# Performance work log

Hardware: AMD Instinct MI355X
Metric: run time of the kernel (lower is better)

## Reference

```python
import jax, jax.numpy as jnp
import numpy as np

N_USERS, N_ITEMS = 100000, 50000
DIM = 128
E_U, E_I = 400000, 200000
B = 4096


def _init_layer(key, dim):
    k1, k2, k3 = jax.random.split(key, 3)
    s = 1.0 / np.sqrt(dim)
    W = jax.random.uniform(k1, (dim, dim), jnp.float32, -s, s)
    a_src = jax.random.uniform(k2, (dim,), jnp.float32, -s, s)
    a_dst = jax.random.uniform(k3, (dim,), jnp.float32, -s, s)
    return W, a_src, a_dst


def setup_inputs() -> dict:
    key = jax.random.key(0)
    ks = jax.random.split(key, 12)
    inp = {
        "uedg_index": jax.random.randint(ks[0], (2, E_U), 0, N_USERS),
        "iedg_index": jax.random.randint(ks[1], (2, E_I), 0, N_ITEMS),
        "user_id": jax.random.randint(ks[2], (B,), 0, N_USERS),
        "item_id": jax.random.randint(ks[3], (B,), 0, N_ITEMS),
        "uedg_value": jax.random.uniform(ks[4], (E_U,), jnp.float32),
        "iedg_value": jax.random.uniform(ks[5], (E_I,), jnp.float32),
        # learned parameters (t.rand init in the original)
        "user_matrix": jax.random.uniform(ks[6], (N_USERS, DIM), jnp.float32),
        "item_matrix": jax.random.uniform(ks[7], (N_ITEMS, DIM), jnp.float32),
    }
    for name, k in (("u1", ks[8]), ("u2", ks[9]), ("i1", ks[10]), ("i2", ks[11])):
        W, a_s, a_d = _init_layer(k, DIM)
        inp[f"W_{name}"] = W
        inp[f"a_src_{name}"] = a_s
        inp[f"a_dst_{name}"] = a_d
    return inp


def gat_layer(x, edge_index, edge_value, W, a_src, a_dst):
    """Single-head GAT layer with per-edge weights (dropout disabled / eval mode)."""
    n = x.shape[0]
    h = x @ W                                   # [N, D]
    src, dst = edge_index[0], edge_index[1]
    hs, hd = h[src], h[dst]                     # [E, D] gathers
    logits = jax.nn.leaky_relu((hs * a_src).sum(-1) + (hd * a_dst).sum(-1), 0.2)  # [E]
    # numerically-stable neighbor softmax over destination nodes
    m = jax.ops.segment_max(logits, dst, num_segments=n)
    e = jnp.exp(logits - m[dst]) * edge_value
    denom = jax.ops.segment_sum(e, dst, num_segments=n)
    coef = e / (denom[dst] + 1e-16)
    out = jax.ops.segment_sum(hs * coef[:, None], dst, num_segments=n)  # scatter-add aggregation
    return jax.nn.elu(out)


def reference(uedg_index, iedg_index, user_id, item_id, uedg_value, iedg_value,
              user_matrix, item_matrix,
              W_u1, a_src_u1, a_dst_u1, W_u2, a_src_u2, a_dst_u2,
              W_i1, a_src_i1, a_dst_i1, W_i2, a_src_i2, a_dst_i2):
    iout = gat_layer(item_matrix, iedg_index, iedg_value, W_i1, a_src_i1, a_dst_i1)
    uout = gat_layer(user_matrix, uedg_index, uedg_value, W_u1, a_src_u1, a_dst_u1)
    iout = gat_layer(iout, iedg_index, iedg_value, W_i2, a_src_i2, a_dst_i2)
    uout = gat_layer(uout, uedg_index, uedg_value, W_u2, a_src_u2, a_dst_u2)
    user_vc = uout[user_id]   # index_select over rows
    item_vc = iout[item_id]
    return user_vc, item_vc
```

## Files before the change

kernel.cpp:

```cpp
#include <hip/hip_runtime.h>
#include <hip/hip_bf16.h>

#define DIM 128
#define KSEG 32

typedef short bf16x8 __attribute__((ext_vector_type(8)));
typedef float f32x4  __attribute__((ext_vector_type(4)));

__device__ __forceinline__ float elu_f(float x) { return x > 0.f ? x : expm1f(x); }

__device__ __forceinline__ unsigned short f2bfu(float f) {
    return __builtin_bit_cast(unsigned short, __float2bfloat16(f));
}
__device__ __forceinline__ float bf2f(unsigned short b) {
    return __uint_as_float(((unsigned)b) << 16);
}

struct PrepArgs {
    const float* W[4];
    const float* as[4];
    const float* ad[4];
    unsigned short* Wt;
    unsigned short* wa;
};

__global__ __launch_bounds__(256) void init_all(int* __restrict__ z, int n, PrepArgs p, int nz)
{
    const int t = threadIdx.x;
    if ((int)blockIdx.x < nz) {
        int i = blockIdx.x * 256 + t;
        if (i < n) z[i] = 0;
        return;
    }
    __shared__ float as[DIM], ad[DIM];
    __shared__ float sr[4][2];
    const int pb    = blockIdx.x - nz;
    const int layer = pb >> 3;
    const int blk   = pb & 7;
    const float* W  = p.W[layer];
    unsigned short* W_t = p.Wt + layer * DIM * DIM;
    unsigned short* wa  = p.wa + layer * 2 * DIM;
    if (t < DIM) as[t] = p.as[layer][t];
    else ad[t - DIM] = p.ad[layer][t - DIM];
    __syncthreads();
    const int half = t >> 7;
    const int c = t & 127;
    const int wv = t >> 6;
    const int k_end = blk * 16 + 16;
    for (int k0 = blk * 16; k0 < k_end; k0 += 2) {
        const int k = k0 + half;
        float w = W[k * DIM + c];
        W_t[c * DIM + k] = f2bfu(w);
        float vs = w * as[c], vd = w * ad[c];
#pragma unroll
        for (int o = 32; o > 0; o >>= 1) { vs += __shfl_down(vs, o); vd += __shfl_down(vd, o); }
        if ((t & 63) == 0) { sr[wv][0] = vs; sr[wv][1] = vd; }
        __syncthreads();
        if (t < 2) {
            const int kk = k0 + t;
            wa[kk]       = f2bfu(sr[2 * t][0] + sr[2 * t + 1][0]);
            wa[DIM + kk] = f2bfu(sr[2 * t][1] + sr[2 * t + 1][1]);
        }
        __syncthreads();
    }
}

__global__ __launch_bounds__(256) void mark_isB(const int* __restrict__ uid, const int* __restrict__ iid,
                                                int B, int NU, int* __restrict__ isB, int* __restrict__ flag)
{
    int ent = blockIdx.x * 256 + threadIdx.x;
    if (ent >= 2 * B) return;
    int n = (ent < B) ? uid[ent] : NU + iid[ent - B];
    isB[n] = 1;
    flag[n] = 1;
}

__global__ __launch_bounds__(256) void pass1_gemm(
    const int* __restrict__ ued, const int* __restrict__ ied,
    const float* __restrict__ uval, const float* __restrict__ ival,
    int EU, int EI, const int* __restrict__ isB, int* __restrict__ flag,
    int* __restrict__ cnt, int2* __restrict__ epair,
    const float* __restrict__ xu, const float* __restrict__ xi,
    const unsigned short* __restrict__ Wt_u, const unsigned short* __restrict__ Wt_i,
    const unsigned short* __restrict__ wa_u, const unsigned short* __restrict__ wa_i,
    unsigned short* __restrict__ h, float* __restrict__ s_src, float* __restrict__ s_dst,
    int NU, int NI, int gu)
{
    __shared__ short xs[2][64 * 128];
    const int t = threadIdx.x;

    const int gbid = blockIdx.x;
    const bool isU = gbid < gu;
    const int b0   = isU ? gbid : gbid - gu;
    const int nblk = isU ? gu : (gridDim.x - gu);
    const int Nl   = isU ? NU : NI;
    const int gofs = isU ? 0 : NU;
    const float* xf = isU ? xu : xi;
    const unsigned short* W_t = isU ? Wt_u : Wt_i;
    const unsigned short* wa  = isU ? wa_u : wa_i;
    const int ntiles = (Nl + 63) >> 6;

    int srow[4], suc[4];
#pragma unroll
    for (int i = 0; i < 4; ++i) {
        int unit = i * 256 + t;
        srow[i] = unit >> 4;
        suc[i]  = unit & 15;
    }
    float4 va[4], vb[4];

    auto LOADREGS = [&](int r0) {
#pragma unroll
        for (int i = 0; i < 4; ++i) {
            int gr = r0 + srow[i];
            if (gr < Nl) {
                const float4* p = reinterpret_cast<const float4*>(&xf[(size_t)gr * DIM + suc[i] * 8]);
                va[i] = p[0];
                vb[i] = p[1];
            } else {
                va[i] = make_float4(0.f, 0.f, 0.f, 0.f);
                vb[i] = make_float4(0.f, 0.f, 0.f, 0.f);
            }
        }
    };
    auto STORELDS = [&](int buf) {
#pragma unroll
        for (int i = 0; i < 4; ++i) {
            bf16x8 bv;
            bv[0] = (short)f2bfu(va[i].x); bv[1] = (short)f2bfu(va[i].y);
            bv[2] = (short)f2bfu(va[i].z); bv[3] = (short)f2bfu(va[i].w);
            bv[4] = (short)f2bfu(vb[i].x); bv[5] = (short)f2bfu(vb[i].y);
            bv[6] = (short)f2bfu(vb[i].z); bv[7] = (short)f2bfu(vb[i].w);
            int byte = srow[i] * 256 + ((suc[i] * 16) ^ ((srow[i] & 7) << 4));
            *reinterpret_cast<bf16x8*>(reinterpret_cast<char*>(xs[buf]) + byte) = bv;
        }
    };

    const bool hasTile = b0 < ntiles;
    if (hasTile) LOADREGS(b0 * 64);

    {
        const int ET = EU + EI;
        const int stride = gridDim.x * 256;
        int e0 = gbid * 256 + t;
        int nd[4], sv[4]; float vv[4]; int ib[4];
#pragma unroll
        for (int j = 0; j < 4; ++j) {
            int e = e0 + j * stride;
            nd[j] = -1;
            if (e < ET) {
                if (e < EU) { nd[j] = ued[EU + e]; sv[j] = ued[e]; vv[j] = uval[e]; }
                else { int ee = e - EU; nd[j] = NU + ied[EI + ee]; sv[j] = NU + ied[ee]; vv[j] = ival[ee]; }
            }
        }
#pragma unroll
        for (int j = 0; j < 4; ++j)
            ib[j] = (nd[j] >= 0) ? isB[nd[j]] : 0;
#pragma unroll
        for (int j = 0; j < 4; ++j) {
            if (ib[j]) {
                int rk = atomicAdd(&cnt[nd[j]], 1);
                if (rk < KSEG)
                    epair[(size_t)nd[j] * KSEG + rk] = make_int2(sv[j], __float_as_int(vv[j]));
                flag[sv[j]] = 1;
            }
        }
    }

    if (!hasTile) return;

    const int wv = t >> 6;
    const int l  = t & 63;
    const int lo = l & 15;
    const int hi = l >> 4;

    bf16x8 wf[4][2];
#pragma unroll
    for (int cb2 = 0; cb2 < 2; ++cb2) {
        const unsigned short* base = W_t + (wv * 32 + cb2 * 16 + lo) * DIM + hi * 8;
#pragma unroll
        for (int kb = 0; kb < 4; ++kb)
            wf[kb][cb2] = *reinterpret_cast<const bf16x8*>(base + kb * 32);
    }
    bf16x8 sfrag[4];
    if (lo < 2) {
        const unsigned short* sb = wa + lo * DIM + hi * 8;
#pragma unroll
        for (int kb = 0; kb < 4; ++kb)
            sfrag[kb] = *reinterpret_cast<const bf16x8*>(sb + kb * 32);
    } else {
#pragma unroll
        for (int kb = 0; kb < 4; ++kb) {
            bf16x8 z = { 0, 0, 0, 0, 0, 0, 0, 0 };
            sfrag[kb] = z;
        }
    }

    int tile = b0;
    STORELDS(0);
    __syncthreads();
    int cur = 0;
    for (;;) {
        const int nextTile = tile + nblk;
        const bool more = nextTile < ntiles;
        if (more) LOADREGS(nextTile * 64);

        const int r0 = tile * 64;
#pragma unroll
        for (int rb = 0; rb < 4; ++rb) {
            const int arow = rb * 16 + lo;
            bf16x8 a[4];
#pragma unroll
            for (int kb = 0; kb < 4; ++kb) {
                int byte = arow * 256 + ((kb * 64 + hi * 16) ^ ((arow & 7) << 4));
                a[kb] = *reinterpret_cast<const bf16x8*>(reinterpret_cast<const char*>(xs[cur]) + byte);
            }
            f32x4 acc0 = {0.f,0.f,0.f,0.f}, acc1 = {0.f,0.f,0.f,0.f};
#pragma unroll
            for (int kb = 0; kb < 4; ++kb) {
                acc0 = __builtin_amdgcn_mfma_f32_16x16x32_bf16(a[kb], wf[kb][0], acc0, 0, 0, 0);
                acc1 = __builtin_amdgcn_mfma_f32_16x16x32_bf16(a[kb], wf[kb][1], acc1, 0, 0, 0);
            }
#pragma unroll
            for (int i = 0; i < 4; ++i) {
                int row = r0 + rb * 16 + hi * 4 + i;
                if (row < Nl) {
                    size_t grow = (size_t)(gofs + row);
                    h[grow * DIM + wv * 32 + lo]      = f2bfu(acc0[i]);
                    h[grow * DIM + wv * 32 + 16 + lo] = f2bfu(acc1[i]);
                }
            }
            if (rb == wv) {
                f32x4 acc_s = {0.f,0.f,0.f,0.f};
#pragma unroll
                for (int kb = 0; kb < 4; ++kb)
                    acc_s = __builtin_amdgcn_mfma_f32_16x16x32_bf16(a[kb], sfrag[kb], acc_s, 0, 0, 0);
#pragma unroll
                for (int i = 0; i < 4; ++i) {
                    int row = r0 + wv * 16 + hi * 4 + i;
                    if (row < Nl) {
                        if (lo == 0) s_src[gofs + row] = acc_s[i];
                        else if (lo == 1) s_dst[gofs + row] = acc_s[i];
                    }
                }
            }
        }

        if (!more) break;
        STORELDS(cur ^ 1);
        __syncthreads();
        cur ^= 1;
        tile = nextTile;
    }
}

__global__ __launch_bounds__(256) void pass2_scan(
    const int* __restrict__ ued, const int* __restrict__ ied,
    const float* __restrict__ uval, const float* __restrict__ ival,
    int EU, int EI, const int* __restrict__ isB, const int* __restrict__ flag,
    int* __restrict__ cnt, int2* __restrict__ epair, int gP,
    int NT, int* __restrict__ aux, int NU)
{
    const int t = threadIdx.x;
    if ((int)blockIdx.x < gP) {
        const int ET = EU + EI;
        const int stride = gP * 256;
        int e0 = blockIdx.x * 256 + t;
        int nd[4], sv[4]; float vv[4]; int act[4];
#pragma unroll
        for (int j = 0; j < 4; ++j) {
            int e = e0 + j * stride;
            nd[j] = -1;
            if (e < ET) {
                if (e < EU) { nd[j] = ued[EU + e]; sv[j] = ued[e]; vv[j] = uval[e]; }
                else { int ee = e - EU; nd[j] = NU + ied[EI + ee]; sv[j] = NU + ied[ee]; vv[j] = ival[ee]; }
            }
        }
#pragma unroll
        for (int j = 0; j < 4; ++j)
            act[j] = (nd[j] >= 0) ? (flag[nd[j]] && !isB[nd[j]]) : 0;
#pragma unroll
        for (int j = 0; j < 4; ++j) {
            if (act[j]) {
                int rk = atomicAdd(&cnt[nd[j]], 1);
                if (rk < KSEG)
                    epair[(size_t)nd[j] * KSEG + rk] = make_int2(sv[j], __float_as_int(vv[j]));
            }
        }
        return;
    }
    __shared__ int sm[4];
    int i = (blockIdx.x - gP) * 256 + t;
    int v = (i < NT) ? flag[i] : 0;
#pragma unroll
    for (int o = 32; o > 0; o >>= 1) v += __shfl_down(v, o);
    if ((t & 63) == 0) sm[t >> 6] = v;
    __syncthreads();
    if (t == 0) aux[blockIdx.x - gP] = sm[0] + sm[1] + sm[2] + sm[3];
}

__global__ __launch_bounds__(256) void scan_build(const int* __restrict__ flag, const int* __restrict__ aux,
                                                  int NT, int NU, int nb,
                                                  int* __restrict__ alist, int* __restrict__ cpos,
                                                  int* __restrict__ hdr)
{
    __shared__ int s[256];
    __shared__ int sm[16];
    const int t = threadIdx.x;
    const int b = blockIdx.x;
    const int i = b * 256 + t;
    int v = (i < NT) ? flag[i] : 0;
    s[t] = v;
    __syncthreads();
    for (int o = 1; o < 256; o <<= 1) {
        int u = (t >= o) ? s[t - o] : 0;
        __syncthreads();
        s[t] += u;
        __syncthreads();
    }

    const int bNU = NU >> 8, oNU = NU & 255;
    int pb = 0, pn = 0, pt = 0;
    for (int j = t; j < nb; j += 256) {
        int av = aux[j];
        if (j < b)   pb += av;
        if (j < bNU) pn += av;
        pt += av;
    }
#pragma unroll
    for (int o = 32; o > 0; o >>= 1) {
        pb += __shfl_down(pb, o);
        pn += __shfl_down(pn, o);
        pt += __shfl_down(pt, o);
    }
    int r = (t < oNU) ? flag[bNU * 256 + t] : 0;
#pragma unroll
    for (int o = 32; o > 0; o >>= 1) r += __shfl_down(r, o);
    if ((t & 63) == 0) {
        int w = t >> 6;
        sm[w] = pb; sm[4 + w] = pn; sm[8 + w] = pt; sm[12 + w] = r;
    }
    __syncthreads();
    const int exb = sm[0] + sm[1] + sm[2] + sm[3];
    const int nau = sm[4] + sm[5] + sm[6] + sm[7] + sm[12] + sm[13] + sm[14] + sm[15];
    const int na  = sm[8] + sm[9] + sm[10] + sm[11];
    const int nau_pad = (nau + 63) & ~63;
    const int nap = nau_pad + (na - nau);
    const int excl = exb + s[t] - v;

    if (i < NT && v) {
        int pos = (i < NU) ? excl : nau_pad + (excl - nau);
        alist[pos] = i;
        cpos[i] = pos;
    }
    if (b == 0) {
        if (t == 0) { hdr[0] = nau; hdr[1] = na; }
        if (t < 64) {
            int ss = nau + t;
            if (ss < nau_pad) alist[ss] = -1;
        } else if (t < 128) {
            alist[nap + (t - 64)] = -1;
        }
    }
}

__global__ __launch_bounds__(256) void csr_agg_act(const int* __restrict__ cnt, const int2* __restrict__ epair,
                                                   const float* __restrict__ ssrc, const float* __restrict__ sdst,
                                                   const unsigned short* __restrict__ h,
                                                   unsigned short* __restrict__ outb,
                                                   const int* __restrict__ alist, const int* __restrict__ hdr)
{
    const int nau = hdr[0], na = hdr[1];
    const int nap = ((nau + 63) & ~63) + (na - nau);
    int g = (blockIdx.x * 256 + threadIdx.x) >> 4;
    int l16 = threadIdx.x & 15;
    if (g >= nap) return;
    int n = alist[g];
    if (n < 0) return;
    const size_t beg = (size_t)n * KSEG;
    int md = min(cnt[n], KSEG);
    float sd = sdst[n];
    float m = -INFINITY, den = 0.f;
    float acc[8] = {0,0,0,0,0,0,0,0};
    for (int base = 0; base < md; base += 16) {
        int c16 = min(16, md - base);
        int sidx = 0; float l = -INFINITY, evv = 0.f;
        if (l16 < c16) {
            int2 pr = epair[beg + base + l16];
            sidx = pr.x;
            evv = __int_as_float(pr.y);
            float ll = ssrc[sidx] + sd;
            l = ll >= 0.f ? ll : 0.2f * ll;
        }
        float cm = l;
#pragma unroll
        for (int o = 8; o > 0; o >>= 1) cm = fmaxf(cm, __shfl_xor(cm, o, 16));
        float nm = fmaxf(m, cm);
        float sc = __expf(m - nm);
        den *= sc;
#pragma unroll
        for (int j = 0; j < 8; ++j) acc[j] *= sc;
        float p = (l16 < c16) ? __expf(l - nm) * evv : 0.f;
        float ps = p;
#pragma unroll
        for (int o = 8; o > 0; o >>= 1) ps += __shfl_xor(ps, o, 16);
        den += ps;
        for (int k0 = 0; k0 < c16; k0 += 4) {
            bf16x8 hv[4]; float cc[4];
#pragma unroll
            for (int j = 0; j < 4; ++j) {
                int k = k0 + j;
                cc[j] = 0.f;
                if (k < c16) {
                    cc[j] = __shfl(p, k, 16);
                    int s = __shfl(sidx, k, 16);
                    hv[j] = *reinterpret_cast<const bf16x8*>(&h[(size_t)s * DIM + l16 * 8]);
                }
            }
#pragma unroll
            for (int j = 0; j < 4; ++j) {
                if (k0 + j < c16) {
#pragma unroll
                    for (int q = 0; q < 8; ++q)
                        acc[q] = fmaf(bf2f((unsigned short)hv[j][q]), cc[j], acc[q]);
                }
            }
        }
        m = nm;
    }
    float inv = 1.f / (den + 1e-16f);
    bf16x8 o;
#pragma unroll
    for (int q = 0; q < 8; ++q) o[q] = (short)f2bfu(elu_f(acc[q] * inv));
    *reinterpret_cast<bf16x8*>(&outb[(size_t)n * DIM + l16 * 8]) = o;
}

__global__ __launch_bounds__(256) void gemm_act(const unsigned short* __restrict__ xbb,
                                                const unsigned short* __restrict__ Wt_u,
                                                const unsigned short* __restrict__ Wt_i,
                                                const unsigned short* __restrict__ wa_u,
                                                const unsigned short* __restrict__ wa_i,
                                                unsigned short* __restrict__ h, float* __restrict__ s_src,
                                                float* __restrict__ s_dst,
                                                const int* __restrict__ alist, const int* __restrict__ hdr)
{
    const int nau = hdr[0], na = hdr[1];
    const int nau_pad = (nau + 63) & ~63;
    const int nap = nau_pad + (na - nau);
    const int r0 = blockIdx.x * 64;
    if (r0 >= nap) return;

    __shared__ short xs[64 * 128];
    __shared__ int rowid[64];
    const int t  = threadIdx.x;
    const int wv = t >> 6;
    const int l  = t & 63;
    const int lo = l & 15;
    const int hi = l >> 4;

    const bool isU = r0 < nau_pad;
    const unsigned short* W_t = isU ? Wt_u : Wt_i;
    const unsigned short* wa  = isU ? wa_u : wa_i;

    if (t < 64) rowid[t] = alist[r0 + t];
    __syncthreads();

    bf16x8 wf[4][2];
#pragma unroll
    for (int cb2 = 0; cb2 < 2; ++cb2) {
        const unsigned short* base = W_t + (wv * 32 + cb2 * 16 + lo) * DIM + hi * 8;
#pragma unroll
        for (int kb = 0; kb < 4; ++kb)
            wf[kb][cb2] = *reinterpret_cast<const bf16x8*>(base + kb * 32);
    }
    bf16x8 sfrag[4];
    if (lo < 2) {
        const unsigned short* sb = wa + lo * DIM + hi * 8;
#pragma unroll
        for (int kb = 0; kb < 4; ++kb)
            sfrag[kb] = *reinterpret_cast<const bf16x8*>(sb + kb * 32);
    } else {
#pragma unroll
        for (int kb = 0; kb < 4; ++kb) {
            bf16x8 z = { 0, 0, 0, 0, 0, 0, 0, 0 };
            sfrag[kb] = z;
        }
    }

#pragma unroll
    for (int i = 0; i < 4; ++i) {
        int unit = i * 256 + t;
        int row = unit >> 4, uc = unit & 15;
        int node = rowid[row];
        bf16x8 bv = { 0, 0, 0, 0, 0, 0, 0, 0 };
        if (node >= 0)
            bv = *reinterpret_cast<const bf16x8*>(&xbb[(size_t)node * DIM + uc * 8]);
        int byte = row * 256 + ((uc * 16) ^ ((row & 7) << 4));
        *reinterpret_cast<bf16x8*>(reinterpret_cast<char*>(xs) + byte) = bv;
    }
    __syncthreads();

#pragma unroll
    for (int rb = 0; rb < 4; ++rb) {
        const int arow = rb * 16 + lo;
        bf16x8 a[4];
#pragma unroll
        for (int kb = 0; kb < 4; ++kb) {
            int byte = arow * 256 + ((kb * 64 + hi * 16) ^ ((arow & 7) << 4));
            a[kb] = *reinterpret_cast<const bf16x8*>(reinterpret_cast<const char*>(xs) + byte);
        }
        f32x4 acc0 = {0.f,0.f,0.f,0.f}, acc1 = {0.f,0.f,0.f,0.f};
#pragma unroll
        for (int kb = 0; kb < 4; ++kb) {
            acc0 = __builtin_amdgcn_mfma_f32_16x16x32_bf16(a[kb], wf[kb][0], acc0, 0, 0, 0);
            acc1 = __builtin_amdgcn_mfma_f32_16x16x32_bf16(a[kb], wf[kb][1], acc1, 0, 0, 0);
        }
#pragma unroll
        for (int i = 0; i < 4; ++i) {
            int row = rb * 16 + hi * 4 + i;
            if (rowid[row] >= 0) {
                size_t grow = (size_t)(r0 + row);
                h[grow * DIM + wv * 32 + lo]      = f2bfu(acc0[i]);
                h[grow * DIM + wv * 32 + 16 + lo] = f2bfu(acc1[i]);
            }
        }
        if (rb == wv) {
            f32x4 acc_s = {0.f,0.f,0.f,0.f};
#pragma unroll
            for (int kb = 0; kb < 4; ++kb)
                acc_s = __builtin_amdgcn_mfma_f32_16x16x32_bf16(a[kb], sfrag[kb], acc_s, 0, 0, 0);
#pragma unroll
            for (int i = 0; i < 4; ++i) {
                int row = wv * 16 + hi * 4 + i;
                if (rowid[row] >= 0) {
                    if (lo == 0) s_src[r0 + row] = acc_s[i];
                    else if (lo == 1) s_dst[r0 + row] = acc_s[i];
                }
            }
        }
    }
}

__global__ __launch_bounds__(256) void csr_agg_batch(const int* __restrict__ cnt, const int2* __restrict__ epair,
                                                     const float* __restrict__ ssrc, const float* __restrict__ sdst,
                                                     const unsigned short* __restrict__ h,
                                                     const int* __restrict__ cpos,
                                                     const int* __restrict__ uid, const int* __restrict__ iid,
                                                     float* __restrict__ out, int B, int NU)
{
    int ent = (blockIdx.x * 256 + threadIdx.x) >> 4;
    int l16 = threadIdx.x & 15;
    if (ent >= 2 * B) return;
    int n = (ent < B) ? uid[ent] : NU + iid[ent - B];
    const size_t beg = (size_t)n * KSEG;
    int md = min(cnt[n], KSEG);
    float sd = sdst[cpos[n]];
    float m = -INFINITY, den = 0.f;
    float acc[8] = {0,0,0,0,0,0,0,0};
    for (int base = 0; base < md; base += 16) {
        int c16 = min(16, md - base);
        int cps = 0; float l = -INFINITY, evv = 0.f;
        if (l16 < c16) {
            int2 pr = epair[beg + base + l16];
            cps = cpos[pr.x];
            evv = __int_as_float(pr.y);
            float ll = ssrc[cps] + sd;
            l = ll >= 0.f ? ll : 0.2f * ll;
        }
        float cm = l;
#pragma unroll
        for (int o = 8; o > 0; o >>= 1) cm = fmaxf(cm, __shfl_xor(cm, o, 16));
        float nm = fmaxf(m, cm);
        float sc = __expf(m - nm);
        den *= sc;
#pragma unroll
        for (int j = 0; j < 8; ++j) acc[j] *= sc;
        float p = (l16 < c16) ? __expf(l - nm) * evv : 0.f;
        float ps = p;
#pragma unroll
        for (int o = 8; o > 0; o >>= 1) ps += __shfl_xor(ps, o, 16);
        den += ps;
        for (int k0 = 0; k0 < c16; k0 += 4) {
            bf16x8 hv[4]; float cc[4];
#pragma unroll
            for (int j = 0; j < 4; ++j) {
                int k = k0 + j;
                cc[j] = 0.f;
                if (k < c16) {
                    cc[j] = __shfl(p, k, 16);
                    int s = __shfl(cps, k, 16);
                    hv[j] = *reinterpret_cast<const bf16x8*>(&h[(size_t)s * DIM + l16 * 8]);
                }
            }
#pragma unroll
            for (int j = 0; j < 4; ++j) {
                if (k0 + j < c16) {
#pragma unroll
                    for (int q = 0; q < 8; ++q)
                        acc[q] = fmaf(bf2f((unsigned short)hv[j][q]), cc[j], acc[q]);
                }
            }
        }
        m = nm;
    }
    float inv = 1.f / (den + 1e-16f);
    float4 o0 = { elu_f(acc[0]*inv), elu_f(acc[1]*inv), elu_f(acc[2]*inv), elu_f(acc[3]*inv) };
    float4 o1 = { elu_f(acc[4]*inv), elu_f(acc[5]*inv), elu_f(acc[6]*inv), elu_f(acc[7]*inv) };
    float4* op = reinterpret_cast<float4*>(&out[(size_t)ent * DIM + l16 * 8]);
    op[0] = o0;
    op[1] = o1;
}

extern "C" void kernel_launch(void* const* d_in, const int* in_sizes, int n_in,
                              void* d_out, int out_size, void* d_ws, size_t ws_size,
                              hipStream_t stream)
{
    const int*   uedg    = (const int*)d_in[0];
    const int*   iedg    = (const int*)d_in[1];
    const int*   user_id = (const int*)d_in[2];
    const int*   item_id = (const int*)d_in[3];
    const float* uval    = (const float*)d_in[4];
    const float* ival    = (const float*)d_in[5];
    const float* umat    = (const float*)d_in[6];
    const float* imat    = (const float*)d_in[7];
    const float* W_u1 = (const float*)d_in[8];
    const float* as_u1 = (const float*)d_in[9];
    const float* ad_u1 = (const float*)d_in[10];
    const float* W_u2 = (const float*)d_in[11];
    const float* as_u2 = (const float*)d_in[12];
    const float* ad_u2 = (const float*)d_in[13];
    const float* W_i1 = (const float*)d_in[14];
    const float* as_i1 = (const float*)d_in[15];
    const float* ad_i1 = (const float*)d_in[16];
    const float* W_i2 = (const float*)d_in[17];
    const float* as_i2 = (const float*)d_in[18];
    const float* ad_i2 = (const float*)d_in[19];

    const int EU = in_sizes[0] / 2;
    const int EI = in_sizes[1] / 2;
    const int B  = in_sizes[2];
    const int NU = in_sizes[6] / DIM;
    const int NI = in_sizes[7] / DIM;
    const int NT = NU + NI;
    const int ET = EU + EI;
    const int nb = (NT + 255) / 256;

    unsigned short* h    = (unsigned short*)d_ws;
    unsigned short* Wt_a = h + (size_t)NT * DIM;
    unsigned short* wa_a = Wt_a + 4 * DIM * DIM;
    unsigned short* xbb  = wa_a + 4 * 2 * DIM;
    float* ssrc   = (float*)(xbb + (size_t)NT * DIM);
    float* sdst   = ssrc + NT;
    int2*  epair  = (int2*)(sdst + NT);
    int*   cnt    = (int*)(epair + (size_t)NT * KSEG);
    int*   flag   = cnt + NT;
    int*   isB    = flag + NT;
    int*   hdr    = isB + NT;
    int*   aux    = hdr + 8;
    int*   alist  = aux + 1024;
    int*   cpos   = alist + (NT + 128);

    PrepArgs pa;
    pa.W[0] = W_u1; pa.W[1] = W_u2; pa.W[2] = W_i1; pa.W[3] = W_i2;
    pa.as[0] = as_u1; pa.as[1] = as_u2; pa.as[2] = as_i1; pa.as[3] = as_i2;
    pa.ad[0] = ad_u1; pa.ad[1] = ad_u2; pa.ad[2] = ad_i1; pa.ad[3] = ad_i2;
    pa.Wt = Wt_a; pa.wa = wa_a;

    const int zn = 3 * NT;
    const int nz = (zn + 255) / 256;
    init_all<<<nz + 32, 256, 0, stream>>>(cnt, zn, pa, nz);

    mark_isB<<<(2 * B + 255) / 256, 256, 0, stream>>>(user_id, item_id, B, NU, isB, flag);

    const int gu = 512, gi = 256;
    pass1_gemm<<<gu + gi, 256, 0, stream>>>(
        uedg, iedg, uval, ival, EU, EI, isB, flag, cnt, epair,
        umat, imat, Wt_a + 0 * DIM * DIM, Wt_a + 2 * DIM * DIM,
        wa_a + 0 * 2 * DIM, wa_a + 2 * 2 * DIM, h, ssrc, sdst, NU, NI, gu);

    const int gP = (ET + 1023) / 1024;
    pass2_scan<<<gP + nb, 256, 0, stream>>>(uedg, iedg, uval, ival, EU, EI, isB, flag, cnt, epair, gP,
                                            NT, aux, NU);

    scan_build<<<nb, 256, 0, stream>>>(flag, aux, NT, NU, nb, alist, cpos, hdr);

    csr_agg_act<<<(NT + 128 + 15) / 16, 256, 0, stream>>>(cnt, epair, ssrc, sdst, h, xbb, alist, hdr);

    gemm_act<<<(NT + 192) / 64, 256, 0, stream>>>(xbb,
        Wt_a + 1 * DIM * DIM, Wt_a + 3 * DIM * DIM, wa_a + 1 * 2 * DIM, wa_a + 3 * 2 * DIM,
        h, ssrc, sdst, alist, hdr);

    csr_agg_batch<<<(2 * B * 16 + 255) / 256, 256, 0, stream>>>(cnt, epair, ssrc, sdst, h, cpos,
        user_id, item_id, (float*)d_out, B, NU);
}
```

Measured before the change: 92.69 us.

## Replace persistent double-buffered projection GEMM with one 128-row tile per block

The first-layer projection kernel no longer loops over 64-row tiles with a register prefetch and double-buffered LDS. Each block now loads a single 128-row tile into one shared buffer and computes it, and the grid is sized to cover all rows. This drops the loop and prefetch bookkeeping and raises the number of blocks in flight for latency hiding. In exchange, per-block register use (8 float4 pairs) grows, there is no overlap between loading and MFMA within a block, and the fused edge-bucketing pass now runs over a larger grid.

```diff
diff --git a/kernel.cpp b/kernel.cpp
--- a/kernel.cpp
+++ b/kernel.cpp
@@ -84,60 +84,41 @@
     const unsigned short* __restrict__ Wt_u, const unsigned short* __restrict__ Wt_i,
     const unsigned short* __restrict__ wa_u, const unsigned short* __restrict__ wa_i,
     unsigned short* __restrict__ h, float* __restrict__ s_src, float* __restrict__ s_dst,
-    int NU, int NI, int gu)
-{
-    __shared__ short xs[2][64 * 128];
+    int NU, int NI, int nbu)
+{
+    __shared__ short xs[128 * 128];
     const int t = threadIdx.x;
 
     const int gbid = blockIdx.x;
-    const bool isU = gbid < gu;
-    const int b0   = isU ? gbid : gbid - gu;
-    const int nblk = isU ? gu : (gridDim.x - gu);
+    const bool isU = gbid < nbu;
+    const int b0   = isU ? gbid : gbid - nbu;
     const int Nl   = isU ? NU : NI;
     const int gofs = isU ? 0 : NU;
     const float* xf = isU ? xu : xi;
     const unsigned short* W_t = isU ? Wt_u : Wt_i;
     const unsigned short* wa  = isU ? wa_u : wa_i;
-    const int ntiles = (Nl + 63) >> 6;
-
-    int srow[4], suc[4];
-#pragma unroll
-    for (int i = 0; i < 4; ++i) {
+    const int r0 = b0 * 128;
+
+    int srow[8], suc[8];
+#pragma unroll
+    for (int i = 0; i < 8; ++i) {
         int unit = i * 256 + t;
         srow[i] = unit >> 4;
         suc[i]  = unit & 15;
     }
-    float4 va[4], vb[4];
-
-    auto LOADREGS = [&](int r0) {
-#pragma unroll
-        for (int i = 0; i < 4; ++i) {
-            int gr = r0 + srow[i];
-            if (gr < Nl) {
-                const float4* p = reinterpret_cast<const float4*>(&xf[(size_t)gr * DIM + suc[i] * 8]);
-                va[i] = p[0];
-                vb[i] = p[1];
-            } else {
-                va[i] = make_float4(0.f, 0.f, 0.f, 0.f);
-                vb[i] = make_float4(0.f, 0.f, 0.f, 0.f);
-            }
-        }
-    };
-    auto STORELDS = [&](int buf) {
-#pragma unroll
-        for (int i = 0; i < 4; ++i) {
-            bf16x8 bv;
-            bv[0] = (short)f2bfu(va[i].x); bv[1] = (short)f2bfu(va[i].y);
-            bv[2] = (short)f2bfu(va[i].z); bv[3] = (short)f2bfu(va[i].w);
-            bv[4] = (short)f2bfu(vb[i].x); bv[5] = (short)f2bfu(vb[i].y);
-            bv[6] = (short)f2bfu(vb[i].z); bv[7] = (short)f2bfu(vb[i].w);
-            int byte = srow[i] * 256 + ((suc[i] * 16) ^ ((srow[i] & 7) << 4));
-            *reinterpret_cast<bf16x8*>(reinterpret_cast<char*>(xs[buf]) + byte) = bv;
-        }
-    };
-
-    const bool hasTile = b0 < ntiles;
-    if (hasTile) LOADREGS(b0 * 64);
+    float4 va[8], vb[8];
+#pragma unroll
+    for (int i = 0; i < 8; ++i) {
+        int gr = r0 + srow[i];
+        if (gr < Nl) {
+            const float4* p = reinterpret_cast<const float4*>(&xf[(size_t)gr * DIM + suc[i] * 8]);
+            va[i] = p[0];
+            vb[i] = p[1];
+        } else {
+            va[i] = make_float4(0.f, 0.f, 0.f, 0.f);
+            vb[i] = make_float4(0.f, 0.f, 0.f, 0.f);
+        }
+    }
 
     {
         const int ET = EU + EI;
@@ -167,8 +148,6 @@
         }
     }
 
-    if (!hasTile) return;
-
     const int wv = t >> 6;
     const int l  = t & 63;
     const int lo = l & 15;
@@ -196,61 +175,56 @@
         }
     }
 
-    int tile = b0;
-    STORELDS(0);
+#pragma unroll
+    for (int i = 0; i < 8; ++i) {
+        bf16x8 bv;
+        bv[0] = (short)f2bfu(va[i].x); bv[1] = (short)f2bfu(va[i].y);
+        bv[2] = (short)f2bfu(va[i].z); bv[3] = (short)f2bfu(va[i].w);
+        bv[4] = (short)f2bfu(vb[i].x); bv[5] = (short)f2bfu(vb[i].y);
+        bv[6] = (short)f2bfu(vb[i].z); bv[7] = (short)f2bfu(vb[i].w);
+        int byte = srow[i] * 256 + ((suc[i] * 16) ^ ((srow[i] & 7) << 4));
+        *reinterpret_cast<bf16x8*>(reinterpret_cast<char*>(xs) + byte) = bv;
+    }
     __syncthreads();
-    int cur = 0;
-    for (;;) {
-        const int nextTile = tile + nblk;
-        const bool more = nextTile < ntiles;
-        if (more) LOADREGS(nextTile * 64);
-
-        const int r0 = tile * 64;
-#pragma unroll
-        for (int rb = 0; rb < 4; ++rb) {
-            const int arow = rb * 16 + lo;
-            bf16x8 a[4];
-#pragma unroll
-            for (int kb = 0; kb < 4; ++kb) {
-                int byte = arow * 256 + ((kb * 64 + hi * 16) ^ ((arow & 7) << 4));
-                a[kb] = *reinterpret_cast<const bf16x8*>(reinterpret_cast<const char*>(xs[cur]) + byte);
-            }
-            f32x4 acc0 = {0.f,0.f,0.f,0.f}, acc1 = {0.f,0.f,0.f,0.f};
-#pragma unroll
-            for (int kb = 0; kb < 4; ++kb) {
-                acc0 = __builtin_amdgcn_mfma_f32_16x16x32_bf16(a[kb], wf[kb][0], acc0, 0, 0, 0);
-                acc1 = __builtin_amdgcn_mfma_f32_16x16x32_bf16(a[kb], wf[kb][1], acc1, 0, 0, 0);
-            }
+
+#pragma unroll
+    for (int rb = 0; rb < 8; ++rb) {
+        const int arow = rb * 16 + lo;
+        bf16x8 a[4];
+#pragma unroll
+        for (int kb = 0; kb < 4; ++kb) {
+            int byte = arow * 256 + ((kb * 64 + hi * 16) ^ ((arow & 7) << 4));
+            a[kb] = *reinterpret_cast<const bf16x8*>(reinterpret_cast<const char*>(xs) + byte);
+        }
+        f32x4 acc0 = {0.f,0.f,0.f,0.f}, acc1 = {0.f,0.f,0.f,0.f};
+#pragma unroll
+        for (int kb = 0; kb < 4; ++kb) {
+            acc0 = __builtin_amdgcn_mfma_f32_16x16x32_bf16(a[kb], wf[kb][0], acc0, 0, 0, 0);
+            acc1 = __builtin_amdgcn_mfma_f32_16x16x32_bf16(a[kb], wf[kb][1], acc1, 0, 0, 0);
+        }
+#pragma unroll
+        for (int i = 0; i < 4; ++i) {
+            int row = r0 + rb * 16 + hi * 4 + i;
+            if (row < Nl) {
+                size_t grow = (size_t)(gofs + row);
+                h[grow * DIM + wv * 32 + lo]      = f2bfu(acc0[i]);
+                h[grow * DIM + wv * 32 + 16 + lo] = f2bfu(acc1[i]);
+            }
+        }
+        if ((rb >> 1) == wv) {
+            f32x4 acc_s = {0.f,0.f,0.f,0.f};
+#pragma unroll
+            for (int kb = 0; kb < 4; ++kb)
+                acc_s = __builtin_amdgcn_mfma_f32_16x16x32_bf16(a[kb], sfrag[kb], acc_s, 0, 0, 0);
 #pragma unroll
             for (int i = 0; i < 4; ++i) {
                 int row = r0 + rb * 16 + hi * 4 + i;
                 if (row < Nl) {
-                    size_t grow = (size_t)(gofs + row);
-                    h[grow * DIM + wv * 32 + lo]      = f2bfu(acc0[i]);
-                    h[grow * DIM + wv * 32 + 16 + lo] = f2bfu(acc1[i]);
+                    if (lo == 0) s_src[gofs + row] = acc_s[i];
+                    else if (lo == 1) s_dst[gofs + row] = acc_s[i];
                 }
             }
-            if (rb == wv) {
-                f32x4 acc_s = {0.f,0.f,0.f,0.f};
-#pragma unroll
-                for (int kb = 0; kb < 4; ++kb)
-                    acc_s = __builtin_amdgcn_mfma_f32_16x16x32_bf16(a[kb], sfrag[kb], acc_s, 0, 0, 0);
-#pragma unroll
-                for (int i = 0; i < 4; ++i) {
-                    int row = r0 + wv * 16 + hi * 4 + i;
-                    if (row < Nl) {
-                        if (lo == 0) s_src[gofs + row] = acc_s[i];
-                        else if (lo == 1) s_dst[gofs + row] = acc_s[i];
-                    }
-                }
-            }
-        }
-
-        if (!more) break;
-        STORELDS(cur ^ 1);
-        __syncthreads();
-        cur ^= 1;
-        tile = nextTile;
+        }
     }
 }
 
@@ -672,11 +646,11 @@
 
     mark_isB<<<(2 * B + 255) / 256, 256, 0, stream>>>(user_id, item_id, B, NU, isB, flag);
 
-    const int gu = 512, gi = 256;
-    pass1_gemm<<<gu + gi, 256, 0, stream>>>(
+    const int nbu = (NU + 127) / 128, nbi = (NI + 127) / 128;
+    pass1_gemm<<<nbu + nbi, 256, 0, stream>>>(
         uedg, iedg, uval, ival, EU, EI, isB, flag, cnt, epair,
         umat, imat, Wt_a + 0 * DIM * DIM, Wt_a + 2 * DIM * DIM,
-        wa_a + 0 * 2 * DIM, wa_a + 2 * 2 * DIM, h, ssrc, sdst, NU, NI, gu);
+        wa_a + 0 * 2 * DIM, wa_a + 2 * 2 * DIM, h, ssrc, sdst, NU, NI, nbu);
 
     const int gP = (ET + 1023) / 1024;
     pass2_scan<<<gP + nb, 256, 0, stream>>>(uedg, iedg, uval, ival, EU, EI, isB, flag, cnt, epair, gP,
```

Measured after the change: 99.29 us. 1.07x slower.
